# Kernel optimization log

Hardware: AMD Instinct MI355X
Metric: run time of the kernel (lower is better)

Reference implementation:

```python
import jax, jax.numpy as jnp
import numpy as np

N, E = 50000, 800000
NFEAT, NHID = 128, 128


def setup_inputs() -> dict:
    key = jax.random.key(0)
    ks = jax.random.split(key, 10)
    s = 1.0 / np.sqrt(NFEAT)
    inp = {
        "x": jax.random.normal(ks[0], (N, NFEAT), dtype=jnp.float32),
        "edge_index": jax.random.randint(ks[1], (2, E), 0, N, dtype=jnp.int32),
        "head": 0,
        # Relation params (nn.Linear weights, [out, in], bias=False)
        "gamma1_w": jax.random.uniform(ks[2], (NFEAT, NFEAT), jnp.float32, -s, s),
        "gamma2_w": jax.random.uniform(ks[3], (NFEAT, NFEAT), jnp.float32, -s, s),
        "beta1_w": jax.random.uniform(ks[4], (NFEAT, NFEAT), jnp.float32, -s, s),
        "beta2_w": jax.random.uniform(ks[5], (NFEAT, NFEAT), jnp.float32, -s, s),
        "r": jax.random.uniform(ks[6], (1, NFEAT), jnp.float32, -s, s),
        # GCNConv params: lin (bias=False) + conv bias
        "lin_w": jax.random.uniform(ks[7], (NHID, NFEAT), jnp.float32, -s, s),
        "bias": jnp.zeros((NHID,), dtype=jnp.float32),
    }
    return inp


def _lrelu(v):
    return jnp.where(v >= 0, v, 0.2 * v)  # LeakyReLU(0.2)


def _forward(x, edge_index, gamma1_w, gamma2_w, beta1_w, beta2_w, r, lin_w, bias):
    n = x.shape[0]
    row, col = edge_index[0], edge_index[1]
    ones_e = jnp.ones((edge_index.shape[1],), dtype=x.dtype)

    # num_neighbor = scatter_add(ones, row); neighbor = scatter_mean(x[col], row)
    num_neighbor = jax.ops.segment_sum(ones_e, row, num_segments=n)  # [N]
    neigh_sum = jax.ops.segment_sum(x[col], row, num_segments=n)      # [N, F]
    neighbor = neigh_sum / jnp.maximum(num_neighbor, 1.0)[:, None]

    # Relation (ablation=0): FiLM-style translation vector
    gamma = _lrelu(x @ gamma1_w.T + neighbor @ gamma2_w.T) + 1.0
    beta = _lrelu(x @ beta1_w.T + neighbor @ beta2_w.T)
    output = x + (gamma * r + beta) - neighbor                        # [N, F]

    xw = x @ lin_w.T                                                  # [N, H]
    loop = jnp.arange(n, dtype=row.dtype)
    row2 = jnp.concatenate([row, loop])
    col2 = jnp.concatenate([col, loop])
    deg = jax.ops.segment_sum(jnp.ones_like(row2, dtype=x.dtype), col2, num_segments=n)
    dinv = jnp.where(deg > 0, jax.lax.rsqrt(deg), 0.0)
    norm = dinv[row2] * dinv[col2]                                    # [E+N]
    h_k = jax.ops.segment_sum(norm[:, None] * xw[row2], col2, num_segments=n) + bias

    # tail branch (head=False, ablation=0): h_s = output, projected by gc.lin.weight
    h_s = output @ lin_w.T
    h_k = (h_k + h_s) / (num_neighbor + 1.0)[:, None]
    return h_k, output


def reference(x, edge_index, head, gamma1_w, gamma2_w, beta1_w, beta2_w, r, lin_w, bias):
    # head is a static Python int (0 -> tail branch, the full fused path)
    assert not head
    return _forward(x, edge_index, gamma1_w, gamma2_w, beta1_w, beta2_w, r, lin_w, bias)
```

## Files before the change

### kernel.cpp

```cpp
#include <hip/hip_runtime.h>

#define NN 50000
#define NE 800000
#define NF 128

#define SHIFT 8
#define NB 196
#define PBLOCKS 128
#define PCHUNK ((NE + PBLOCKS - 1) / PBLOCKS)

#define NTILES ((NN + 63) / 64)
#define FBLOCKS 512

#define CVX_BLOCKS 3125
#define CVW_BLOCKS 320
#define PREP_BLOCKS (CVX_BLOCKS + CVW_BLOCKS + PBLOCKS)

typedef __attribute__((ext_vector_type(4))) float f32x4;
typedef __attribute__((ext_vector_type(8))) short bf16x8;

__device__ __forceinline__ short f2bf(float f) {
    unsigned u = __float_as_uint(f);
    u += 0x7FFF + ((u >> 16) & 1);
    return (short)(u >> 16);
}
__device__ __forceinline__ float bf2f(short s) {
    return __uint_as_float(((unsigned)(unsigned short)s) << 16);
}

__global__ __launch_bounds__(256) void prep_kernel(
    const float* __restrict__ x, const float* __restrict__ g1,
    const float* __restrict__ g2, const float* __restrict__ b1,
    const float* __restrict__ b2, const float* __restrict__ lin,
    const int* __restrict__ ei, short* __restrict__ xbf,
    short* __restrict__ wbf, int* __restrict__ gcnt) {
    __shared__ int cnt[2 * NB];
    int bid = blockIdx.x;
    int t = threadIdx.x;

    if (bid < CVX_BLOCKS) {
        int i = bid * 256 + t;
        if (i < NN * NF / 8) {
            float4 a = ((const float4*)x)[i * 2];
            float4 b = ((const float4*)x)[i * 2 + 1];
            bf16x8 v;
            v[0] = f2bf(a.x); v[1] = f2bf(a.y); v[2] = f2bf(a.z); v[3] = f2bf(a.w);
            v[4] = f2bf(b.x); v[5] = f2bf(b.y); v[6] = f2bf(b.z); v[7] = f2bf(b.w);
            *(bf16x8*)(xbf + i * 8) = v;
        }
        return;
    }
    if (bid < CVX_BLOCKS + CVW_BLOCKS) {
        int i = (bid - CVX_BLOCKS) * 256 + t;
        if (i < 5 * NF * NF) {
            int m = i >> 14, off = i & (NF * NF - 1);
            float v = (m == 0) ? g1[off] : (m == 1) ? g2[off] : (m == 2) ? b1[off]
                    : (m == 3) ? b2[off] : lin[off];
            wbf[i] = f2bf(v);
        }
        return;
    }
    int pb = bid - CVX_BLOCKS - CVW_BLOCKS;
    for (int i = t; i < 2 * NB; i += 256) cnt[i] = 0;
    __syncthreads();
    int lo = pb * PCHUNK;
    int hi = min(lo + PCHUNK, NE);
    for (int j = lo + t; j < hi; j += 256) {
        int r = ei[j];
        int c = ei[NE + j];
        atomicAdd(&cnt[r >> SHIFT], 1);
        atomicAdd(&cnt[NB + (c >> SHIFT)], 1);
    }
    __syncthreads();
    for (int i = t; i < 2 * NB; i += 256)
        if (cnt[i]) atomicAdd(&gcnt[i], cnt[i]);
}

__global__ __launch_bounds__(256) void p1_scan_kernel(const int* __restrict__ gcnt,
                                                      int* __restrict__ baseR,
                                                      int* __restrict__ baseC,
                                                      int* __restrict__ gcur) {
    __shared__ int s[256];
    int t = threadIdx.x;
    int v = (t < NB) ? gcnt[t] : 0;
    s[t] = v;
    __syncthreads();
    for (int off = 1; off < 256; off <<= 1) {
        int u = (t >= off) ? s[t - off] : 0;
        __syncthreads();
        s[t] += u;
        __syncthreads();
    }
    if (t < NB) {
        int excl = s[t] - v;
        baseR[t] = excl;
        gcur[t] = excl;
        if (t == NB - 1) baseR[NB] = s[t];
    }
    __syncthreads();
    int v2 = (t < NB) ? gcnt[NB + t] : 0;
    s[t] = v2;
    __syncthreads();
    for (int off = 1; off < 256; off <<= 1) {
        int u = (t >= off) ? s[t - off] : 0;
        __syncthreads();
        s[t] += u;
        __syncthreads();
    }
    if (t < NB) {
        int excl = s[t] - v2;
        baseC[t] = excl;
        gcur[NB + t] = excl;
        if (t == NB - 1) baseC[NB] = s[t];
    }
}

__global__ __launch_bounds__(256) void p2_partition_kernel(const int* __restrict__ ei,
                                                           int* __restrict__ gcur,
                                                           unsigned* __restrict__ partR,
                                                           unsigned* __restrict__ partC) {
    __shared__ int cnt[2 * NB];
    __shared__ int res[2 * NB];
    int t = threadIdx.x;
    for (int i = t; i < 2 * NB; i += 256) cnt[i] = 0;
    __syncthreads();
    int lo = blockIdx.x * PCHUNK;
    int hi = min(lo + PCHUNK, NE);
    for (int j = lo + t; j < hi; j += 256) {
        int r = ei[j];
        int c = ei[NE + j];
        atomicAdd(&cnt[r >> SHIFT], 1);
        atomicAdd(&cnt[NB + (c >> SHIFT)], 1);
    }
    __syncthreads();
    for (int i = t; i < 2 * NB; i += 256) {
        int n = cnt[i];
        res[i] = n ? atomicAdd(&gcur[i], n) : 0;
        cnt[i] = 0;
    }
    __syncthreads();
    for (int j = lo + t; j < hi; j += 256) {
        int r = ei[j];
        int c = ei[NE + j];
        int bR = r >> SHIFT;
        int sR = atomicAdd(&cnt[bR], 1);
        partR[res[bR] + sR] = ((unsigned)(r & 255) << 17) | (unsigned)c;
        int bC = NB + (c >> SHIFT);
        int sC = atomicAdd(&cnt[bC], 1);
        partC[res[bC] + sC] = ((unsigned)(c & 255) << 17) | (unsigned)r;
    }
}

__global__ __launch_bounds__(256) void p3_build_kernel(
    const unsigned* __restrict__ partR, const unsigned* __restrict__ partC,
    const int* __restrict__ baseR, const int* __restrict__ baseC,
    int* __restrict__ offs_r, int* __restrict__ offs_c,
    int* __restrict__ csr_r, int* __restrict__ csr_c,
    int* __restrict__ degr, float* __restrict__ dinv) {
    int side = blockIdx.x / NB;
    int b = blockIdx.x - side * NB;
    const unsigned* part = side ? partC : partR;
    const int* base = side ? baseC : baseR;
    int* offs = side ? offs_c : offs_r;
    int* csr = side ? csr_c : csr_r;

    __shared__ int deg[256];
    __shared__ int cur[256];
    int t = threadIdx.x;
    int s0 = base[b], s1 = base[b + 1];
    deg[t] = 0;
    __syncthreads();
    for (int j = s0 + t; j < s1; j += 256)
        atomicAdd(&deg[part[j] >> 17], 1);
    __syncthreads();
    int myDeg = deg[t];
    for (int off = 1; off < 256; off <<= 1) {
        int u = (t >= off) ? deg[t - off] : 0;
        __syncthreads();
        deg[t] += u;
        __syncthreads();
    }
    int excl = deg[t] - myDeg;
    int node = (b << SHIFT) + t;
    if (node <= NN) offs[node] = s0 + excl;
    if (node < NN) {
        if (side == 0) degr[node] = myDeg;
        else           dinv[node] = rsqrtf((float)myDeg + 1.0f);
    }
    cur[t] = excl;
    __syncthreads();
    for (int j = s0 + t; j < s1; j += 256) {
        unsigned en = part[j];
        int k = en >> 17;
        int p = atomicAdd(&cur[k], 1);
        csr[s0 + p] = (int)(en & 0x1FFFFu);
    }
}

__global__ __launch_bounds__(256) void gather_fused_kernel(
    const int* __restrict__ offs_r, const int* __restrict__ csr_r,
    const int* __restrict__ offs_c, const int* __restrict__ csr_c,
    const short* __restrict__ xbf, const float* __restrict__ dinv,
    short* __restrict__ nbbf, short* __restrict__ zbf) {
    int g = blockIdx.x * 16 + (threadIdx.x >> 4);
    int l = threadIdx.x & 15;
    if (g >= NN) return;
    const short* xb = xbf + l * 8;

    int s = offs_r[g], e = offs_r[g + 1];
    float acc[8] = {0.f, 0.f, 0.f, 0.f, 0.f, 0.f, 0.f, 0.f};
    int j = s;
    for (; j + 4 <= e; j += 4) {
        int s0 = csr_r[j], s1 = csr_r[j + 1], s2 = csr_r[j + 2], s3 = csr_r[j + 3];
        bf16x8 v0 = *(const bf16x8*)(xb + s0 * NF);
        bf16x8 v1 = *(const bf16x8*)(xb + s1 * NF);
        bf16x8 v2 = *(const bf16x8*)(xb + s2 * NF);
        bf16x8 v3 = *(const bf16x8*)(xb + s3 * NF);
        #pragma unroll
        for (int k = 0; k < 8; ++k)
            acc[k] += (bf2f(v0[k]) + bf2f(v1[k])) + (bf2f(v2[k]) + bf2f(v3[k]));
    }
    for (; j < e; ++j) {
        bf16x8 v = *(const bf16x8*)(xb + csr_r[j] * NF);
        #pragma unroll
        for (int k = 0; k < 8; ++k) acc[k] += bf2f(v[k]);
    }
    float invn = 1.0f / fmaxf((float)(e - s), 1.0f);
    bf16x8 o;
    #pragma unroll
    for (int k = 0; k < 8; ++k) o[k] = f2bf(acc[k] * invn);
    *(bf16x8*)(nbbf + g * NF + l * 8) = o;

    s = offs_c[g]; e = offs_c[g + 1];
    float az[8] = {0.f, 0.f, 0.f, 0.f, 0.f, 0.f, 0.f, 0.f};
    j = s;
    for (; j + 4 <= e; j += 4) {
        int s0 = csr_c[j], s1 = csr_c[j + 1], s2 = csr_c[j + 2], s3 = csr_c[j + 3];
        float w0 = dinv[s0], w1 = dinv[s1], w2 = dinv[s2], w3 = dinv[s3];
        bf16x8 v0 = *(const bf16x8*)(xb + s0 * NF);
        bf16x8 v1 = *(const bf16x8*)(xb + s1 * NF);
        bf16x8 v2 = *(const bf16x8*)(xb + s2 * NF);
        bf16x8 v3 = *(const bf16x8*)(xb + s3 * NF);
        #pragma unroll
        for (int k = 0; k < 8; ++k)
            az[k] += (w0 * bf2f(v0[k]) + w1 * bf2f(v1[k]))
                   + (w2 * bf2f(v2[k]) + w3 * bf2f(v3[k]));
    }
    for (; j < e; ++j) {
        int s0 = csr_c[j];
        float w0 = dinv[s0];
        bf16x8 v = *(const bf16x8*)(xb + s0 * NF);
        #pragma unroll
        for (int k = 0; k < 8; ++k) az[k] += w0 * bf2f(v[k]);
    }
    float dc = dinv[g];
    bf16x8 self = *(const bf16x8*)(xb + g * NF);
    bf16x8 zo;
    #pragma unroll
    for (int k = 0; k < 8; ++k) zo[k] = f2bf(dc * (az[k] + dc * bf2f(self[k])));
    *(bf16x8*)(zbf + g * NF + l * 8) = zo;
}

__global__ __launch_bounds__(256, 2) void film_mfma_kernel(
    const short* __restrict__ xbf, const short* __restrict__ nbbf,
    const short* __restrict__ zbf, const short* __restrict__ wbf,
    const float* __restrict__ rvec, const float* __restrict__ bias,
    const int* __restrict__ degr, float* __restrict__ outp,
    float* __restrict__ hko) {
    __shared__ short xs[64 * NF];
    __shared__ short ns[64 * NF];
    __shared__ short zs[64 * NF];

    int tid = threadIdx.x;
    int w = tid >> 6;
    int l = tid & 63;
    int lr = l & 15;
    int lg = l >> 4;

    bf16x8 wf[2][5][4];
    float rc[2], bc[2];
    #pragma unroll
    for (int j = 0; j < 2; ++j) {
        int col = (2 * w + j) * 16 + lr;
        #pragma unroll
        for (int m = 0; m < 5; ++m) {
            const short* wm = wbf + m * 16384 + col * NF;
            #pragma unroll
            for (int kb = 0; kb < 4; ++kb)
                wf[j][m][kb] = *(const bf16x8*)(wm + kb * 32 + lg * 8);
        }
        rc[j] = rvec[col];
        bc[j] = bias[col];
    }

    #pragma unroll 1
    for (int tile = blockIdx.x; tile < NTILES; tile += FBLOCKS) {
        int node0 = tile * 64;

        #pragma unroll
        for (int it = 0; it < 4; ++it) {
            int chunk = it * 256 + tid;
            int row = chunk >> 4;
            int c = chunk & 15;
            int grow = min(node0 + row, NN - 1);
            int swz = ((c ^ (row & 7)) << 3);
            *(bf16x8*)(xs + row * NF + swz) = *(const bf16x8*)(xbf + grow * NF + c * 8);
            *(bf16x8*)(ns + row * NF + swz) = *(const bf16x8*)(nbbf + grow * NF + c * 8);
            *(bf16x8*)(zs + row * NF + swz) = *(const bf16x8*)(zbf + grow * NF + c * 8);
        }
        __syncthreads();

        #pragma unroll 1
        for (int rg = 0; rg < 4; ++rg) {
            bf16x8 xf[4], nf[4];
            #pragma unroll
            for (int kb = 0; kb < 4; ++kb) {
                int row = rg * 16 + lr;
                int swz = (((kb * 4 + lg) ^ (row & 7)) << 3);
                xf[kb] = *(const bf16x8*)(xs + row * NF + swz);
                nf[kb] = *(const bf16x8*)(ns + row * NF + swz);
            }
            #pragma unroll
            for (int j = 0; j < 2; ++j) {
                f32x4 ag = {0.f, 0.f, 0.f, 0.f};
                f32x4 ab = {0.f, 0.f, 0.f, 0.f};
                #pragma unroll
                for (int kb = 0; kb < 4; ++kb) {
                    ag = __builtin_amdgcn_mfma_f32_16x16x32_bf16(xf[kb], wf[j][0][kb], ag, 0, 0, 0);
                    ag = __builtin_amdgcn_mfma_f32_16x16x32_bf16(nf[kb], wf[j][1][kb], ag, 0, 0, 0);
                    ab = __builtin_amdgcn_mfma_f32_16x16x32_bf16(xf[kb], wf[j][2][kb], ab, 0, 0, 0);
                    ab = __builtin_amdgcn_mfma_f32_16x16x32_bf16(nf[kb], wf[j][3][kb], ab, 0, 0, 0);
                }
                int col = (2 * w + j) * 16 + lr;
                #pragma unroll
                for (int q = 0; q < 4; ++q) {
                    int nl = rg * 16 + lg * 4 + q;
                    int ng = node0 + nl;
                    int addr = nl * NF + (((col >> 3) ^ (nl & 7)) << 3) + (col & 7);
                    float xv = bf2f(xs[addr]);
                    float nv = bf2f(ns[addr]);
                    float gp = ag[q], bp = ab[q];
                    float gamma = (gp >= 0.f ? gp : 0.2f * gp) + 1.0f;
                    float beta  = (bp >= 0.f ? bp : 0.2f * bp);
                    float o = xv + gamma * rc[j] + beta - nv;
                    if (ng < NN) outp[ng * NF + col] = o;
                    zs[addr] = f2bf(o + bf2f(zs[addr]));
                }
            }
        }
        __syncthreads();

        #pragma unroll 1
        for (int rg = 0; rg < 4; ++rg) {
            bf16x8 of[4];
            #pragma unroll
            for (int kb = 0; kb < 4; ++kb) {
                int row = rg * 16 + lr;
                int swz = (((kb * 4 + lg) ^ (row & 7)) << 3);
                of[kb] = *(const bf16x8*)(zs + row * NF + swz);
            }
            float invdq[4];
            #pragma unroll
            for (int q = 0; q < 4; ++q)
                invdq[q] = 1.0f / ((float)degr[min(node0 + rg * 16 + lg * 4 + q, NN - 1)] + 1.0f);
            #pragma unroll
            for (int j = 0; j < 2; ++j) {
                f32x4 as = {0.f, 0.f, 0.f, 0.f};
                #pragma unroll
                for (int kb = 0; kb < 4; ++kb)
                    as = __builtin_amdgcn_mfma_f32_16x16x32_bf16(of[kb], wf[j][4][kb], as, 0, 0, 0);
                int col = (2 * w + j) * 16 + lr;
                #pragma unroll
                for (int q = 0; q < 4; ++q) {
                    int ng = node0 + rg * 16 + lg * 4 + q;
                    if (ng < NN) hko[ng * NF + col] = (as[q] + bc[j]) * invdq[q];
                }
            }
        }
        __syncthreads();
    }
}

extern "C" void kernel_launch(void* const* d_in, const int* in_sizes, int n_in,
                              void* d_out, int out_size, void* d_ws, size_t ws_size,
                              hipStream_t stream) {
    const float* x    = (const float*)d_in[0];
    const int*   ei   = (const int*)d_in[1];
    const float* g1   = (const float*)d_in[3];
    const float* g2   = (const float*)d_in[4];
    const float* b1   = (const float*)d_in[5];
    const float* b2   = (const float*)d_in[6];
    const float* rv   = (const float*)d_in[7];
    const float* lin  = (const float*)d_in[8];
    const float* bias = (const float*)d_in[9];

    float* dinv = (float*)d_ws;
    int* degr   = (int*)(dinv + NN);
    int* offs_r = degr + NN;
    int* offs_c = offs_r + (NN + 1);
    int* csr_r  = offs_c + (NN + 1);
    int* csr_c  = csr_r + NE;
    unsigned* partR = (unsigned*)(csr_c + NE);
    unsigned* partC = partR + NE;
    int* gcnt   = (int*)(partC + NE);
    int* gcur   = gcnt + 2 * NB;
    int* baseR  = gcur + 2 * NB;
    int* baseC  = baseR + (NB + 1);
    uintptr_t p = (uintptr_t)(baseC + NB + 1);
    p = (p + 15) & ~(uintptr_t)15;
    short* xbf  = (short*)p;
    short* nbbf = xbf + NN * NF;
    short* zbf  = nbbf + NN * NF;
    short* wbf  = zbf + NN * NF;

    float* hko  = (float*)d_out;
    float* outp = hko + NN * NF;

    hipMemsetAsync(gcnt, 0, 2 * NB * sizeof(int), stream);

    prep_kernel<<<PREP_BLOCKS, 256, 0, stream>>>(x, g1, g2, b1, b2, lin, ei,
                                                 xbf, wbf, gcnt);
    p1_scan_kernel<<<1, 256, 0, stream>>>(gcnt, baseR, baseC, gcur);
    p2_partition_kernel<<<PBLOCKS, 256, 0, stream>>>(ei, gcur, partR, partC);
    p3_build_kernel<<<2 * NB, 256, 0, stream>>>(partR, partC, baseR, baseC,
                                                offs_r, offs_c, csr_r, csr_c, degr, dinv);
    gather_fused_kernel<<<(NN + 15) / 16, 256, 0, stream>>>(offs_r, csr_r, offs_c, csr_c,
                                                            xbf, dinv, nbbf, zbf);
    film_mfma_kernel<<<FBLOCKS, 256, 0, stream>>>(xbf, nbbf, zbf, wbf, rv, bias, degr,
                                                  outp, hko);
}
```

Measured before the change: 173.8 us.

## Split bf16 feature arrays into four column quarters for cache-local gathers

The bf16 copies of x, the neighbor mean and the GCN aggregate are stored as four separate 32-column slabs instead of row-major 128-column rows. The gather kernel launches four times as many blocks, one per quarter, and spreads each node's edges over four lanes that are combined with shuffles. Each gather pass therefore touches a working set a quarter the size, which is meant to raise L2/MALL hit rates for random neighbor reads. In exchange the edge index lists and dinv are read four times, and each gathered row segment is only 64 bytes.

Result: no change. 172.5 us (-0.7%).

```diff
diff --git a/kernel.cpp b/kernel.cpp
--- a/kernel.cpp
+++ b/kernel.cpp
@@ -3,6 +3,7 @@
 #define NN 50000
 #define NE 800000
 #define NF 128
+#define QS (NN * 32)
 
 #define SHIFT 8
 #define NB 196
@@ -32,7 +33,7 @@
     const float* __restrict__ x, const float* __restrict__ g1,
     const float* __restrict__ g2, const float* __restrict__ b1,
     const float* __restrict__ b2, const float* __restrict__ lin,
-    const int* __restrict__ ei, short* __restrict__ xbf,
+    const int* __restrict__ ei, short* __restrict__ xq,
     short* __restrict__ wbf, int* __restrict__ gcnt) {
     __shared__ int cnt[2 * NB];
     int bid = blockIdx.x;
@@ -40,13 +41,15 @@
 
     if (bid < CVX_BLOCKS) {
         int i = bid * 256 + t;
-        if (i < NN * NF / 8) {
+        if (i < NN * 16) {
+            int n = i >> 4, c = i & 15;
+            int q = c >> 2, sub = c & 3;
             float4 a = ((const float4*)x)[i * 2];
             float4 b = ((const float4*)x)[i * 2 + 1];
             bf16x8 v;
             v[0] = f2bf(a.x); v[1] = f2bf(a.y); v[2] = f2bf(a.z); v[3] = f2bf(a.w);
             v[4] = f2bf(b.x); v[5] = f2bf(b.y); v[6] = f2bf(b.z); v[7] = f2bf(b.w);
-            *(bf16x8*)(xbf + i * 8) = v;
+            *(bf16x8*)(xq + (size_t)q * QS + n * 32 + sub * 8) = v;
         }
         return;
     }
@@ -200,70 +203,80 @@
 __global__ __launch_bounds__(256) void gather_fused_kernel(
     const int* __restrict__ offs_r, const int* __restrict__ csr_r,
     const int* __restrict__ offs_c, const int* __restrict__ csr_c,
-    const short* __restrict__ xbf, const float* __restrict__ dinv,
-    short* __restrict__ nbbf, short* __restrict__ zbf) {
-    int g = blockIdx.x * 16 + (threadIdx.x >> 4);
-    int l = threadIdx.x & 15;
-    if (g >= NN) return;
-    const short* xb = xbf + l * 8;
+    const short* __restrict__ xq, const float* __restrict__ dinv,
+    short* __restrict__ nbq, short* __restrict__ zq) {
+    int q = blockIdx.x & 3;
+    int grp = blockIdx.x >> 2;
+    int t = threadIdx.x;
+    int g = grp * 16 + (t >> 4);
+    int slot = (t >> 2) & 3;
+    int fl = t & 3;
+    const short* xb = xq + (size_t)q * QS + fl * 8;
 
     int s = offs_r[g], e = offs_r[g + 1];
     float acc[8] = {0.f, 0.f, 0.f, 0.f, 0.f, 0.f, 0.f, 0.f};
-    int j = s;
-    for (; j + 4 <= e; j += 4) {
-        int s0 = csr_r[j], s1 = csr_r[j + 1], s2 = csr_r[j + 2], s3 = csr_r[j + 3];
-        bf16x8 v0 = *(const bf16x8*)(xb + s0 * NF);
-        bf16x8 v1 = *(const bf16x8*)(xb + s1 * NF);
-        bf16x8 v2 = *(const bf16x8*)(xb + s2 * NF);
-        bf16x8 v3 = *(const bf16x8*)(xb + s3 * NF);
-        #pragma unroll
-        for (int k = 0; k < 8; ++k)
-            acc[k] += (bf2f(v0[k]) + bf2f(v1[k])) + (bf2f(v2[k]) + bf2f(v3[k]));
-    }
-    for (; j < e; ++j) {
-        bf16x8 v = *(const bf16x8*)(xb + csr_r[j] * NF);
+    int j = s + slot;
+    for (; j + 4 < e; j += 8) {
+        int s0 = csr_r[j], s1 = csr_r[j + 4];
+        bf16x8 v0 = *(const bf16x8*)(xb + s0 * 32);
+        bf16x8 v1 = *(const bf16x8*)(xb + s1 * 32);
+        #pragma unroll
+        for (int k = 0; k < 8; ++k) acc[k] += bf2f(v0[k]) + bf2f(v1[k]);
+    }
+    for (; j < e; j += 4) {
+        bf16x8 v = *(const bf16x8*)(xb + csr_r[j] * 32);
         #pragma unroll
         for (int k = 0; k < 8; ++k) acc[k] += bf2f(v[k]);
     }
-    float invn = 1.0f / fmaxf((float)(e - s), 1.0f);
-    bf16x8 o;
     #pragma unroll
-    for (int k = 0; k < 8; ++k) o[k] = f2bf(acc[k] * invn);
-    *(bf16x8*)(nbbf + g * NF + l * 8) = o;
+    for (int k = 0; k < 8; ++k) {
+        acc[k] += __shfl_xor(acc[k], 4);
+        acc[k] += __shfl_xor(acc[k], 8);
+    }
+    if (slot == 0) {
+        float invn = 1.0f / fmaxf((float)(e - s), 1.0f);
+        bf16x8 o;
+        #pragma unroll
+        for (int k = 0; k < 8; ++k) o[k] = f2bf(acc[k] * invn);
+        *(bf16x8*)(nbq + (size_t)q * QS + g * 32 + fl * 8) = o;
+    }
 
     s = offs_c[g]; e = offs_c[g + 1];
     float az[8] = {0.f, 0.f, 0.f, 0.f, 0.f, 0.f, 0.f, 0.f};
-    j = s;
-    for (; j + 4 <= e; j += 4) {
-        int s0 = csr_c[j], s1 = csr_c[j + 1], s2 = csr_c[j + 2], s3 = csr_c[j + 3];
-        float w0 = dinv[s0], w1 = dinv[s1], w2 = dinv[s2], w3 = dinv[s3];
-        bf16x8 v0 = *(const bf16x8*)(xb + s0 * NF);
-        bf16x8 v1 = *(const bf16x8*)(xb + s1 * NF);
-        bf16x8 v2 = *(const bf16x8*)(xb + s2 * NF);
-        bf16x8 v3 = *(const bf16x8*)(xb + s3 * NF);
-        #pragma unroll
-        for (int k = 0; k < 8; ++k)
-            az[k] += (w0 * bf2f(v0[k]) + w1 * bf2f(v1[k]))
-                   + (w2 * bf2f(v2[k]) + w3 * bf2f(v3[k]));
-    }
-    for (; j < e; ++j) {
+    j = s + slot;
+    for (; j + 4 < e; j += 8) {
+        int s0 = csr_c[j], s1 = csr_c[j + 4];
+        float w0 = dinv[s0], w1 = dinv[s1];
+        bf16x8 v0 = *(const bf16x8*)(xb + s0 * 32);
+        bf16x8 v1 = *(const bf16x8*)(xb + s1 * 32);
+        #pragma unroll
+        for (int k = 0; k < 8; ++k) az[k] += w0 * bf2f(v0[k]) + w1 * bf2f(v1[k]);
+    }
+    for (; j < e; j += 4) {
         int s0 = csr_c[j];
         float w0 = dinv[s0];
-        bf16x8 v = *(const bf16x8*)(xb + s0 * NF);
+        bf16x8 v = *(const bf16x8*)(xb + s0 * 32);
         #pragma unroll
         for (int k = 0; k < 8; ++k) az[k] += w0 * bf2f(v[k]);
     }
-    float dc = dinv[g];
-    bf16x8 self = *(const bf16x8*)(xb + g * NF);
-    bf16x8 zo;
     #pragma unroll
-    for (int k = 0; k < 8; ++k) zo[k] = f2bf(dc * (az[k] + dc * bf2f(self[k])));
-    *(bf16x8*)(zbf + g * NF + l * 8) = zo;
+    for (int k = 0; k < 8; ++k) {
+        az[k] += __shfl_xor(az[k], 4);
+        az[k] += __shfl_xor(az[k], 8);
+    }
+    if (slot == 0) {
+        float dc = dinv[g];
+        bf16x8 self = *(const bf16x8*)(xb + g * 32);
+        bf16x8 zo;
+        #pragma unroll
+        for (int k = 0; k < 8; ++k) zo[k] = f2bf(dc * (az[k] + dc * bf2f(self[k])));
+        *(bf16x8*)(zq + (size_t)q * QS + g * 32 + fl * 8) = zo;
+    }
 }
 
 __global__ __launch_bounds__(256, 2) void film_mfma_kernel(
-    const short* __restrict__ xbf, const short* __restrict__ nbbf,
-    const short* __restrict__ zbf, const short* __restrict__ wbf,
+    const short* __restrict__ xq, const short* __restrict__ nbq,
+    const short* __restrict__ zq, const short* __restrict__ wbf,
     const float* __restrict__ rvec, const float* __restrict__ bias,
     const int* __restrict__ degr, float* __restrict__ outp,
     float* __restrict__ hko) {
@@ -304,9 +317,10 @@
             int c = chunk & 15;
             int grow = min(node0 + row, NN - 1);
             int swz = ((c ^ (row & 7)) << 3);
-            *(bf16x8*)(xs + row * NF + swz) = *(const bf16x8*)(xbf + grow * NF + c * 8);
-            *(bf16x8*)(ns + row * NF + swz) = *(const bf16x8*)(nbbf + grow * NF + c * 8);
-            *(bf16x8*)(zs + row * NF + swz) = *(const bf16x8*)(zbf + grow * NF + c * 8);
+            size_t qoff = (size_t)(c >> 2) * QS + grow * 32 + (c & 3) * 8;
+            *(bf16x8*)(xs + row * NF + swz) = *(const bf16x8*)(xq + qoff);
+            *(bf16x8*)(ns + row * NF + swz) = *(const bf16x8*)(nbq + qoff);
+            *(bf16x8*)(zs + row * NF + swz) = *(const bf16x8*)(zq + qoff);
         }
         __syncthreads();
 
@@ -408,10 +422,10 @@
     int* baseC  = baseR + (NB + 1);
     uintptr_t p = (uintptr_t)(baseC + NB + 1);
     p = (p + 15) & ~(uintptr_t)15;
-    short* xbf  = (short*)p;
-    short* nbbf = xbf + NN * NF;
-    short* zbf  = nbbf + NN * NF;
-    short* wbf  = zbf + NN * NF;
+    short* xq   = (short*)p;
+    short* nbq  = xq + 4 * QS;
+    short* zq   = nbq + 4 * QS;
+    short* wbf  = zq + 4 * QS;
 
     float* hko  = (float*)d_out;
     float* outp = hko + NN * NF;
@@ -419,13 +433,13 @@
     hipMemsetAsync(gcnt, 0, 2 * NB * sizeof(int), stream);
 
     prep_kernel<<<PREP_BLOCKS, 256, 0, stream>>>(x, g1, g2, b1, b2, lin, ei,
-                                                 xbf, wbf, gcnt);
+                                                 xq, wbf, gcnt);
     p1_scan_kernel<<<1, 256, 0, stream>>>(gcnt, baseR, baseC, gcur);
     p2_partition_kernel<<<PBLOCKS, 256, 0, stream>>>(ei, gcur, partR, partC);
     p3_build_kernel<<<2 * NB, 256, 0, stream>>>(partR, partC, baseR, baseC,
                                                 offs_r, offs_c, csr_r, csr_c, degr, dinv);
-    gather_fused_kernel<<<(NN + 15) / 16, 256, 0, stream>>>(offs_r, csr_r, offs_c, csr_c,
-                                                            xbf, dinv, nbbf, zbf);
-    film_mfma_kernel<<<FBLOCKS, 256, 0, stream>>>(xbf, nbbf, zbf, wbf, rv, bias, degr,
+    gather_fused_kernel<<<(NN / 16) * 4, 256, 0, stream>>>(offs_r, csr_r, offs_c, csr_c,
+                                                           xq, dinv, nbq, zq);
+    film_mfma_kernel<<<FBLOCKS, 256, 0, stream>>>(xq, nbq, zq, wbf, rv, bias, degr,
                                                   outp, hko);
 }
```
